# Performance work log

Hardware: AMD Instinct MI355X
Metric: run time of the kernel (lower is better)

Reference implementation:

```python
import jax, jax.numpy as jnp
import numpy as np

N, L, E_Q, E_TOTAL, H, FORECAST = 4, 2048, 512, 512, 8, 8
E_HEAD = E_TOTAL // H
DT = 1.0
NEG = -1e30


def setup_inputs() -> dict:
    rng = jax.random.key(0)
    ks = jax.random.split(rng, 8)
    inv = 1.0 / np.sqrt(E_Q)
    return {
        "query": jax.random.normal(ks[0], (N, L, E_Q), jnp.float32),
        "key": jax.random.normal(ks[1], (N, L, E_Q), jnp.float32),
        "value": jax.random.normal(ks[2], (N, L, E_Q), jnp.float32),
        "Wqkv": jax.random.normal(ks[3], (E_Q, 3 * E_TOTAL), jnp.float32) * inv,
        "bqkv": jnp.zeros((3 * E_TOTAL,), jnp.float32),
        "Wo": jax.random.normal(ks[4], (E_TOTAL, E_Q), jnp.float32) * (1.0 / np.sqrt(E_TOTAL)),
        "bo": jnp.zeros((E_Q,), jnp.float32),
        "Xi": jax.random.normal(ks[5], (H, E_HEAD, E_HEAD), jnp.float32) * 0.02,
    }


def reference(query, key, value, Wqkv, bqkv, Wo, bo, Xi):
    # NOTE: original forward projects `query` into q,k,v (key/value args unused).
    b, s, _ = query.shape
    qkv = query @ Wqkv + bqkv                      # [b, s, 3E]
    q, k, v = jnp.split(qkv, 3, axis=-1)
    split_heads = lambda t: t.reshape(b, s, H, E_HEAD).transpose(0, 2, 1, 3)  # [b,H,s,h]
    q, k, v = split_heads(q), split_heads(k), split_heads(v)
    # causal SDPA
    scale = 1.0 / np.sqrt(E_HEAD)
    scores = jnp.einsum('bhqd,bhkd->bhqk', q, k) * scale
    causal = jnp.tril(jnp.ones((s, s), bool))
    scores = jnp.where(causal, scores, NEG)
    probs = jax.nn.softmax(scores, axis=-1)
    attn = jnp.einsum('bhqk,bhkd->bhqd', probs, v)  # [b,H,s,h]
    # per-head SINDy linear dynamics, strict symmetry -> skew-symmetric A
    A = Xi - jnp.swapaxes(Xi, -1, -2)               # [H,h,h]

    def step(x, _):
        x2 = x + DT * jnp.einsum('bhsd,hde->bhse', x, A)
        return x2, x2

    _, ys = jax.lax.scan(step, attn, None, length=FORECAST)  # [n,b,H,s,h]
    roll = jnp.transpose(ys, (1, 0, 3, 2, 4)).reshape(b, FORECAST, s, E_TOTAL)
    return roll @ Wo + bo                            # [b, n, s, E_q]
```

## Files before the change

### kernel.cpp

```cpp
#include <hip/hip_runtime.h>
#include <math.h>


#define NEGV -1e30f

typedef __bf16 bf16_t;
typedef __bf16 bf16x4 __attribute__((ext_vector_type(4)));
typedef __bf16 bf16x8 __attribute__((ext_vector_type(8)));
typedef float f32x4 __attribute__((ext_vector_type(4)));

#define MFMA(a, b, c) __builtin_amdgcn_mfma_f32_16x16x32_bf16((a), (b), (c), 0, 0, 0)

#define QSCALE 0.18033688011112042f

__device__ __forceinline__ bf16x8* swz_ptr(bf16_t* base, int r, int cb) {
  return (bf16x8*)((char*)base + r * 128 + (cb ^ ((r & 7) << 4)));
}
__device__ __forceinline__ const bf16x8* swz_cptr(const bf16_t* base, int r, int cb) {
  return (const bf16x8*)((const char*)base + r * 128 + (cb ^ ((r & 7) << 4)));
}

__device__ __forceinline__ void gload16(const bf16_t* g, bf16_t* l) {
  __builtin_amdgcn_global_load_lds(
      (const __attribute__((address_space(1))) void*)g,
      (__attribute__((address_space(3))) void*)l, 16, 0, 0);
}


__global__ __launch_bounds__(256) void xconv(const float* __restrict__ X,
                                             bf16_t* __restrict__ Xb) {
  const int gid = blockIdx.x * 256 + threadIdx.x;
  const int s = gid >> 6, j = gid & 63;
  const float4* src = (const float4*)(X + (size_t)s * 512 + j * 8);
  const float4 f0 = src[0], f1 = src[1];
  bf16x8 v;
  v[0] = (bf16_t)f0.x; v[1] = (bf16_t)f0.y; v[2] = (bf16_t)f0.z; v[3] = (bf16_t)f0.w;
  v[4] = (bf16_t)f1.x; v[5] = (bf16_t)f1.y; v[6] = (bf16_t)f1.z; v[7] = (bf16_t)f1.w;
  *(bf16x8*)&Xb[(size_t)s * 512 + (j >> 3) * 64 + 8 * ((j & 7) ^ (s & 7))] = v;
}

__global__ __launch_bounds__(256) void wconv(const float* __restrict__ W,
                                             bf16_t* __restrict__ WT) {
  const int n0 = blockIdx.x * 64, k0 = blockIdx.y * 64;
  __shared__ float Wf[64][65];
  const int tid = threadIdx.x;
#pragma unroll
  for (int c = 0; c < 16; ++c) {
    const int idx = tid + c * 256;
    const int kk = idx >> 6, nn = idx & 63;
    Wf[kk][nn] = W[(size_t)(k0 + kk) * 1536 + n0 + nn];
  }
  __syncthreads();
  const int nr = tid >> 2;
  const int jb = (tid & 3) * 2;
#pragma unroll
  for (int t = 0; t < 2; ++t) {
    const int j = jb + t;
    bf16x8 v;
#pragma unroll
    for (int i = 0; i < 8; ++i) v[i] = (bf16_t)Wf[j * 8 + i][nr];
    *(bf16x8*)&WT[(size_t)(n0 + nr) * 512 + k0 + 8 * (j ^ (nr & 7))] = v;
  }
}

__global__ __launch_bounds__(256) void build_powers(const float* __restrict__ Xi,
                                                    float* __restrict__ pows) {
  const int h = blockIdx.x;
  __shared__ __align__(16) float P[64][68];
  __shared__ __align__(16) float cur[64][68];
  const int tid = threadIdx.x;
  const float* xi = Xi + (size_t)h * 4096;
  float* dst = pows + (size_t)h * 8 * 4096;
  for (int idx = tid; idx < 4096; idx += 256) {
    const int i = idx >> 6, j = idx & 63;
    const float p = (i == j ? 1.f : 0.f) + xi[i * 64 + j] - xi[j * 64 + i];
    P[i][j] = p;
    cur[i][j] = p;
    dst[idx] = p;
  }
  __syncthreads();
  const int i = tid >> 2;
  const int j0 = (tid & 3) * 16;
  for (int n = 1; n < 8; ++n) {
    float a[16];
#pragma unroll
    for (int jj = 0; jj < 16; ++jj) a[jj] = 0.f;
    for (int dd = 0; dd < 64; ++dd) {
      const float c = cur[i][dd];
#pragma unroll
      for (int jj = 0; jj < 16; ++jj) a[jj] += c * P[dd][j0 + jj];
    }
    __syncthreads();
#pragma unroll
    for (int jj = 0; jj < 16; ++jj) {
      cur[i][j0 + jj] = a[jj];
      dst[n * 4096 + i * 64 + j0 + jj] = a[jj];
    }
    __syncthreads();
  }
}

__global__ __launch_bounds__(256) void build_B(const float* __restrict__ pows,
                                               const float* __restrict__ Wo,
                                               bf16_t* __restrict__ BmatT) {
  const int et = blockIdx.x;
  const int n = blockIdx.y;
  const int h = blockIdx.z;
  __shared__ __align__(16) float P[64][68];
  __shared__ __align__(16) float We[64][128];
  const int tid = threadIdx.x;
  const float* src = pows + ((size_t)h * 8 + n) * 4096;
  for (int idx = tid; idx < 4096; idx += 256) P[idx >> 6][idx & 63] = src[idx];
  const int e0 = et * 128;
  for (int idx = tid; idx < 8192; idx += 256) {
    const int dd = idx >> 7, e = idx & 127;
    We[dd][e] = Wo[(size_t)(h * 64 + dd) * 512 + e0 + e];
  }
  __syncthreads();
  const int d = tid >> 2;
  const int eq = (tid & 3) * 32;
  float acc[32];
#pragma unroll
  for (int j = 0; j < 32; ++j) acc[j] = 0.f;
  for (int dd = 0; dd < 64; ++dd) {
    const float p = P[d][dd];
#pragma unroll
    for (int j = 0; j < 32; ++j) acc[j] += p * We[dd][eq + j];
  }
  bf16_t* dst = BmatT + (size_t)n * 512 * 512 + (size_t)(e0 + eq) * 512 + h * 64;
  const int dlo = d & 7, dhi = d >> 3;
#pragma unroll
  for (int j = 0; j < 32; ++j)
    dst[(size_t)j * 512 + 8 * (dhi ^ (j & 7)) + dlo] = (bf16_t)acc[j];
}

__global__ __launch_bounds__(256) void qkv_gemm(const bf16_t* __restrict__ Xb,
                                                const bf16_t* __restrict__ WT,
                                                const float* __restrict__ bias,
                                                bf16_t* __restrict__ qw,
                                                bf16_t* __restrict__ kw,
                                                bf16_t* __restrict__ vt) {
  __shared__ __align__(16) bf16_t As[128 * 64];
  __shared__ __align__(16) bf16_t Bs[128 * 64];
  const int tid = threadIdx.x;
  const int wave = tid >> 6, lane = tid & 63;
  const int g = lane >> 4, li = lane & 15;
  const int row0 = blockIdx.x * 128;
  const int col0 = blockIdx.y * 128;
  const int wm = (wave >> 1) * 64, wn = (wave & 1) * 64;
  f32x4 acc[4][4] = {};
  const bf16_t* asrc = Xb + (size_t)(row0 + wave * 32 + (lane >> 3)) * 512 + (lane & 7) * 8;
  const bf16_t* bsrc = WT + (size_t)(col0 + wave * 32 + (lane >> 3)) * 512 + (lane & 7) * 8;
  bf16_t* adst = &As[wave * 32 * 64];
  bf16_t* bdst = &Bs[wave * 32 * 64];
  for (int k0 = 0; k0 < 512; k0 += 64) {
#pragma unroll
    for (int c = 0; c < 4; ++c) {
      gload16(asrc + (size_t)c * 8 * 512 + k0, adst + c * 512);
      gload16(bsrc + (size_t)c * 8 * 512 + k0, bdst + c * 512);
    }
    __syncthreads();
#pragma unroll
    for (int ks = 0; ks < 2; ++ks) {
      bf16x8 af[4], bfr[4];
#pragma unroll
      for (int mr = 0; mr < 4; ++mr)
        af[mr] = *swz_cptr(As, wm + mr * 16 + li, ks * 64 + g * 16);
#pragma unroll
      for (int nr = 0; nr < 4; ++nr)
        bfr[nr] = *swz_cptr(Bs, wn + nr * 16 + li, ks * 64 + g * 16);
#pragma unroll
      for (int mr = 0; mr < 4; ++mr)
#pragma unroll
        for (int nr = 0; nr < 4; ++nr)
          acc[mr][nr] = MFMA(af[mr], bfr[nr], acc[mr][nr]);
    }
    __syncthreads();
  }
  const int cbase = col0 + wn;
  const int sel = cbase >> 9;
  const int hh = (cbase & 511) >> 6;
  const int bb = row0 >> 11;
  const size_t hb = (size_t)(bb * 8 + hh) * (2048 * 64);
  if (sel == 2) {
    bf16_t* vbase = vt + hb;
#pragma unroll
    for (int nr = 0; nr < 4; ++nr) {
      const int dcol = nr * 16 + li;
      const float bv = bias[cbase + dcol];
#pragma unroll
      for (int mr = 0; mr < 4; ++mr) {
        bf16x4 pk;
#pragma unroll
        for (int i = 0; i < 4; ++i) pk[i] = (bf16_t)(acc[mr][nr][i] + bv);
        const int s = (row0 + wm + mr * 16 + g * 4) & 2047;
        *(bf16x4*)&vbase[(size_t)dcol * 2048 + s] = pk;
      }
    }
  } else {
    bf16_t* dstp = (sel == 0 ? qw : kw) + hb;
    const float sc = (sel == 0) ? QSCALE : 1.0f;
#pragma unroll
    for (int nr = 0; nr < 4; ++nr) {
      const int dcol = nr * 16 + li;
      const float bv = bias[cbase + dcol];
#pragma unroll
      for (int mr = 0; mr < 4; ++mr) {
#pragma unroll
        for (int i = 0; i < 4; ++i) {
          const int r = row0 + wm + mr * 16 + g * 4 + i;
          const int s = r & 2047;
          dstp[(size_t)s * 64 + dcol] = (bf16_t)((acc[mr][nr][i] + bv) * sc);
        }
      }
    }
  }
}

__global__ __launch_bounds__(256) void fattn(const bf16_t* __restrict__ qw,
                                             const bf16_t* __restrict__ kw,
                                             const bf16_t* __restrict__ vt,
                                             bf16_t* __restrict__ attn,
                                             float* __restrict__ opart,
                                             float* __restrict__ ml) {
  __shared__ __align__(16) bf16_t Ks[2][64][64];
  __shared__ __align__(16) bf16_t Vs[2][64][64];
  __shared__ __align__(16) bf16_t Ps[4][16][64];
  const int tid = threadIdx.x;
  const int w = tid >> 6;
  const int lane = tid & 63;
  const int g = lane >> 4;
  const int li = lane & 15;
  const int x = blockIdx.x;
  int qt, ktb, kte, chunk;
  bool split;
  if (x < 16) {
    qt = 31 - x; ktb = 0; kte = 16; chunk = 0; split = true;
  } else if (x < 32) {
    qt = 47 - x; ktb = 16; kte = qt + 1; chunk = 1; split = true;
  } else {
    qt = 47 - x; ktb = 0; kte = qt + 1; chunk = 0; split = false;
  }
  const int h = blockIdx.y;
  const int b = blockIdx.z;
  const size_t base = ((size_t)(b * 8 + h)) * (2048 * 64);
  const int q0 = qt * 64;
  const int qrow = q0 + w * 16 + li;
  const bf16x8 aq0 = *(const bf16x8*)(qw + base + (size_t)qrow * 64 + g * 8);
  const bf16x8 aq1 = *(const bf16x8*)(qw + base + (size_t)qrow * 64 + 32 + g * 8);
  const bf16_t* kbase = kw + base;
  const bf16_t* vbase = vt + base;
  const int r_st = tid >> 2;
  const int qu = tid & 3;
  {
    const bf16_t* kp = kbase + (size_t)(ktb * 64 + r_st) * 64 + qu * 16;
    const bf16_t* vp = vbase + (size_t)r_st * 2048 + ktb * 64 + qu * 16;
    *swz_ptr(&Ks[0][0][0], r_st, qu * 32) = *(const bf16x8*)kp;
    *swz_ptr(&Ks[0][0][0], r_st, qu * 32 + 16) = *(const bf16x8*)(kp + 8);
    *swz_ptr(&Vs[0][0][0], r_st, qu * 32) = *(const bf16x8*)vp;
    *swz_ptr(&Vs[0][0][0], r_st, qu * 32 + 16) = *(const bf16x8*)(vp + 8);
  }
  f32x4 accO[4] = {};
  float m_run = -__builtin_inff();
  float l_run = 0.f;
  char* const psrow = (char*)&Ps[w][li][0];
  const int pswz = (li & 7) << 4;
  for (int kt = ktb; kt < kte; ++kt) {
    __syncthreads();
    const int cur = (kt - ktb) & 1;
    const bool pf = (kt + 1) < kte;
    bf16x8 nk0, nk1, nv0, nv1;
    if (pf) {
      const int kb2 = (kt + 1) * 64;
      const bf16_t* kp = kbase + (size_t)(kb2 + r_st) * 64 + qu * 16;
      const bf16_t* vp = vbase + (size_t)r_st * 2048 + kb2 + qu * 16;
      nk0 = *(const bf16x8*)kp;
      nk1 = *(const bf16x8*)(kp + 8);
      nv0 = *(const bf16x8*)vp;
      nv1 = *(const bf16x8*)(vp + 8);
    }
    f32x4 sv[4];
    __builtin_amdgcn_s_setprio(1);
#pragma unroll
    for (int nt = 0; nt < 4; ++nt) {
      const bf16x8 bk0 = *swz_cptr(&Ks[cur][0][0], nt * 16 + li, g * 16);
      const bf16x8 bk1 = *swz_cptr(&Ks[cur][0][0], nt * 16 + li, 64 + g * 16);
      f32x4 z = {0.f, 0.f, 0.f, 0.f};
      z = MFMA(bk0, aq0, z);
      sv[nt] = MFMA(bk1, aq1, z);
    }
    __builtin_amdgcn_s_setprio(0);
    if (kt == qt) {
#pragma unroll
      for (int nt = 0; nt < 4; ++nt)
#pragma unroll
        for (int i = 0; i < 4; ++i)
          if (nt * 16 + g * 4 + i > w * 16 + li) sv[nt][i] = NEGV;
    }
    float pmax = sv[0][0];
#pragma unroll
    for (int nt = 0; nt < 4; ++nt)
#pragma unroll
      for (int i = 0; i < 4; ++i) pmax = fmaxf(pmax, sv[nt][i]);
    pmax = fmaxf(pmax, __shfl_xor(pmax, 16, 64));
    pmax = fmaxf(pmax, __shfl_xor(pmax, 32, 64));
    if (!__all(pmax - m_run <= 8.f)) {
      const float newm = fmaxf(m_run, pmax);
      const float sc = exp2f(m_run - newm);
      l_run *= sc;
      m_run = newm;
#pragma unroll
      for (int nt = 0; nt < 4; ++nt)
#pragma unroll
        for (int i = 0; i < 4; ++i) accO[nt][i] *= sc;
    }
    float rsum = 0.f;
#pragma unroll
    for (int nt = 0; nt < 4; ++nt) {
#pragma unroll
      for (int i = 0; i < 4; ++i) {
        const float p = exp2f(sv[nt][i] - m_run);
        sv[nt][i] = p;
        rsum += p;
      }
    }
    rsum += __shfl_xor(rsum, 16, 64);
    rsum += __shfl_xor(rsum, 32, 64);
    l_run += rsum;
#pragma unroll
    for (int nt = 0; nt < 4; ++nt) {
      bf16x4 pk;
#pragma unroll
      for (int i = 0; i < 4; ++i) pk[i] = (bf16_t)sv[nt][i];
      *(bf16x4*)(psrow + ((nt * 32 + g * 8) ^ pswz)) = pk;
    }
    const bf16x8 ap0 = *(const bf16x8*)(psrow + ((g * 16) ^ pswz));
    const bf16x8 ap1 = *(const bf16x8*)(psrow + ((64 + g * 16) ^ pswz));
    __builtin_amdgcn_s_setprio(1);
#pragma unroll
    for (int nt = 0; nt < 4; ++nt) {
      const bf16x8 bv0 = *swz_cptr(&Vs[cur][0][0], nt * 16 + li, g * 16);
      const bf16x8 bv1 = *swz_cptr(&Vs[cur][0][0], nt * 16 + li, 64 + g * 16);
      accO[nt] = MFMA(bv0, ap0, accO[nt]);
      accO[nt] = MFMA(bv1, ap1, accO[nt]);
    }
    __builtin_amdgcn_s_setprio(0);
    if (pf) {
      *swz_ptr(&Ks[cur ^ 1][0][0], r_st, qu * 32) = nk0;
      *swz_ptr(&Ks[cur ^ 1][0][0], r_st, qu * 32 + 16) = nk1;
      *swz_ptr(&Vs[cur ^ 1][0][0], r_st, qu * 32) = nv0;
      *swz_ptr(&Vs[cur ^ 1][0][0], r_st, qu * 32 + 16) = nv1;
    }
  }
  if (!split) {
    const float inv = 1.0f / l_run;
    bf16_t* arow = attn + (size_t)(b * 2048 + qrow) * 512 + h * 64;
#pragma unroll
    for (int nt = 0; nt < 4; ++nt) {
      bf16x4 pk;
#pragma unroll
      for (int i = 0; i < 4; ++i) pk[i] = (bf16_t)(accO[nt][i] * inv);
      *(bf16x4*)&arow[8 * ((nt * 2 + (g >> 1)) ^ (li & 7)) + (g & 1) * 4] = pk;
    }
  } else {
    const int row = w * 16 + li;
    const size_t pbase = (((size_t)(b * 8 + h) * 16 + (qt - 16)) * 2 + chunk) * 64 + row;
    float* op = opart + pbase * 64;
#pragma unroll
    for (int nt = 0; nt < 4; ++nt) *(f32x4*)&op[nt * 16 + g * 4] = accO[nt];
    if (g == 0) {
      ml[pbase * 2] = m_run;
      ml[pbase * 2 + 1] = l_run;
    }
  }
}

__global__ __launch_bounds__(256) void fcombine(const float* __restrict__ opart,
                                                const float* __restrict__ ml,
                                                bf16_t* __restrict__ attn) {
  const int qi = blockIdx.x;
  const int h = blockIdx.y;
  const int b = blockIdx.z;
  const int tid = threadIdx.x;
  const int row = tid >> 2;
  const int dq = (tid & 3) * 16;
  const size_t base2 = ((size_t)(b * 8 + h) * 16 + qi) * 2;
  const size_t p0 = (base2 * 64 + row);
  const size_t p1 = ((base2 + 1) * 64 + row);
  const float m1 = ml[p0 * 2], l1 = ml[p0 * 2 + 1];
  const float m2 = ml[p1 * 2], l2 = ml[p1 * 2 + 1];
  const float m = fmaxf(m1, m2);
  const float w1 = exp2f(m1 - m), w2 = exp2f(m2 - m);
  const float inv = 1.0f / (l1 * w1 + l2 * w2);
  const float* o1 = opart + p0 * 64;
  const float* o2 = opart + p1 * 64;
  const int qrow = (16 + qi) * 64 + row;
  bf16_t* arow = attn + (size_t)(b * 2048 + qrow) * 512 + h * 64;
#pragma unroll
  for (int t = 0; t < 2; ++t) {
    const int c0 = dq + t * 8;
    const f32x4 a1 = *(const f32x4*)&o1[c0];
    const f32x4 b1 = *(const f32x4*)&o1[c0 + 4];
    const f32x4 a2 = *(const f32x4*)&o2[c0];
    const f32x4 b2 = *(const f32x4*)&o2[c0 + 4];
    bf16x8 v;
#pragma unroll
    for (int i = 0; i < 4; ++i) {
      v[i] = (bf16_t)((a1[i] * w1 + a2[i] * w2) * inv);
      v[4 + i] = (bf16_t)((b1[i] * w1 + b2[i] * w2) * inv);
    }
    *(bf16x8*)&arow[8 * ((c0 >> 3) ^ (row & 7))] = v;
  }
}

__global__ __launch_bounds__(256, 2) void out_gemm(const bf16_t* __restrict__ A,
                                                   const bf16_t* __restrict__ BmatT,
                                                   const float* __restrict__ bo,
                                                   float* __restrict__ out) {
  __shared__ __align__(16) bf16_t As[128 * 64];
  __shared__ __align__(16) bf16_t Bs[2][128 * 64];
  const int tid = threadIdx.x;
  const int wave = tid >> 6, lane = tid & 63;
  const int g = lane >> 4, li = lane & 15;
  const int row0 = blockIdx.x * 128;
  const int col0 = blockIdx.y * 128;
  const int nf0 = blockIdx.z * 2;
  const int wm = (wave >> 1) * 64, wn = (wave & 1) * 64;
  f32x4 acc[2][4][4] = {};
  const bf16_t* asrc = A + (size_t)(row0 + wave * 32 + (lane >> 3)) * 512 + (lane & 7) * 8;
  const bf16_t* bsrc = BmatT + (size_t)nf0 * 512 * 512 +
                       (size_t)(col0 + wave * 32 + (lane >> 3)) * 512 + (lane & 7) * 8;
  bf16_t* adst = &As[wave * 32 * 64];
  bf16_t* bdst0 = &Bs[0][wave * 32 * 64];
  bf16_t* bdst1 = &Bs[1][wave * 32 * 64];
  for (int k0 = 0; k0 < 512; k0 += 64) {
#pragma unroll
    for (int c = 0; c < 4; ++c) {
      gload16(asrc + (size_t)c * 8 * 512 + k0, adst + c * 512);
      gload16(bsrc + (size_t)c * 8 * 512 + k0, bdst0 + c * 512);
      gload16(bsrc + 262144 + (size_t)c * 8 * 512 + k0, bdst1 + c * 512);
    }
    __syncthreads();
#pragma unroll
    for (int ks = 0; ks < 2; ++ks) {
      bf16x8 af[4];
#pragma unroll
      for (int mr = 0; mr < 4; ++mr)
        af[mr] = *swz_cptr(As, wm + mr * 16 + li, ks * 64 + g * 16);
#pragma unroll
      for (int f = 0; f < 2; ++f) {
        bf16x8 bfr[4];
#pragma unroll
        for (int nr = 0; nr < 4; ++nr)
          bfr[nr] = *swz_cptr(Bs[f], wn + nr * 16 + li, ks * 64 + g * 16);
#pragma unroll
        for (int mr = 0; mr < 4; ++mr)
#pragma unroll
          for (int nr = 0; nr < 4; ++nr)
            acc[f][mr][nr] = MFMA(af[mr], bfr[nr], acc[f][mr][nr]);
      }
    }
    __syncthreads();
  }
  const int bb = row0 >> 11;
#pragma unroll
  for (int f = 0; f < 2; ++f) {
    float* obase = out + ((size_t)(bb * 8 + nf0 + f)) * (2048 * 512);
#pragma unroll
    for (int nr = 0; nr < 4; ++nr) {
      const int c = col0 + wn + nr * 16 + li;
      const float bv = bo[c];
#pragma unroll
      for (int mr = 0; mr < 4; ++mr) {
#pragma unroll
        for (int i = 0; i < 4; ++i) {
          const int r = row0 + wm + mr * 16 + g * 4 + i;
          const int s = r & 2047;
          obase[(size_t)s * 512 + c] = acc[f][mr][nr][i] + bv;
        }
      }
    }
  }
}

extern "C" void kernel_launch(void* const* d_in, const int* in_sizes, int n_in,
                              void* d_out, int out_size, void* d_ws, size_t ws_size,
                              hipStream_t stream) {
  const float* query = (const float*)d_in[0];
  const float* Wqkv = (const float*)d_in[3];
  const float* bqkv = (const float*)d_in[4];
  const float* Wo = (const float*)d_in[5];
  const float* bo = (const float*)d_in[6];
  const float* Xi = (const float*)d_in[7];
  float* out = (float*)d_out;

  char* ws = (char*)d_ws;
  bf16_t* qw = (bf16_t*)(ws + 0);
  bf16_t* kw = (bf16_t*)(ws + 8388608);
  bf16_t* vt = (bf16_t*)(ws + 16777216);
  bf16_t* Xb = (bf16_t*)(ws + 25165824);
  bf16_t* attn = (bf16_t*)(ws + 25165824);
  bf16_t* BmatT = (bf16_t*)(ws + 33554432);
  float* pows = (float*)(ws + 37748736);
  bf16_t* WT = (bf16_t*)(ws + 38797312);
  float* opart = (float*)(ws + 40370176);
  float* mlbuf = (float*)(ws + 57147392);

  xconv<<<dim3(2048), dim3(256), 0, stream>>>(query, Xb);
  wconv<<<dim3(24, 8), dim3(256), 0, stream>>>(Wqkv, WT);
  build_powers<<<dim3(8), dim3(256), 0, stream>>>(Xi, pows);
  build_B<<<dim3(4, 8, 8), dim3(256), 0, stream>>>(pows, Wo, BmatT);
  qkv_gemm<<<dim3(64, 12), dim3(256), 0, stream>>>(Xb, WT, bqkv, qw, kw, vt);
  fattn<<<dim3(48, 8, 4), dim3(256), 0, stream>>>(qw, kw, vt, attn, opart, mlbuf);
  fcombine<<<dim3(16, 8, 4), dim3(256), 0, stream>>>(opart, mlbuf, attn);
  out_gemm<<<dim3(64, 4, 4), dim3(256), 0, stream>>>(attn, BmatT, bo, out);
}
```

Before: 185.5 us.

## Double-buffer LDS tiles in qkv and output GEMMs, one forecast step per block

Both GEMMs now use two LDS buffers and prefetch the next K tile with async global-to-LDS loads while the current tile feeds the MFMAs. Explicit vmcnt waits and raw barriers replace __syncthreads. The output GEMM no longer computes two forecast steps per block: each block handles one, so the grid doubles along z and the A tile is loaded twice as often. The aim is to hide global load latency and cut per-thread accumulator pressure, at the cost of more LDS per block and extra A traffic.

```diff
diff --git a/kernel.cpp b/kernel.cpp
--- a/kernel.cpp
+++ b/kernel.cpp
@@ -140,8 +140,8 @@
                                                 bf16_t* __restrict__ qw,
                                                 bf16_t* __restrict__ kw,
                                                 bf16_t* __restrict__ vt) {
-  __shared__ __align__(16) bf16_t As[128 * 64];
-  __shared__ __align__(16) bf16_t Bs[128 * 64];
+  __shared__ __align__(16) bf16_t As[2][128 * 64];
+  __shared__ __align__(16) bf16_t Bs[2][128 * 64];
   const int tid = threadIdx.x;
   const int wave = tid >> 6, lane = tid & 63;
   const int g = lane >> 4, li = lane & 15;
@@ -151,31 +151,49 @@
   f32x4 acc[4][4] = {};
   const bf16_t* asrc = Xb + (size_t)(row0 + wave * 32 + (lane >> 3)) * 512 + (lane & 7) * 8;
   const bf16_t* bsrc = WT + (size_t)(col0 + wave * 32 + (lane >> 3)) * 512 + (lane & 7) * 8;
-  bf16_t* adst = &As[wave * 32 * 64];
-  bf16_t* bdst = &Bs[wave * 32 * 64];
-  for (int k0 = 0; k0 < 512; k0 += 64) {
+  bf16_t* adst0 = &As[0][wave * 32 * 64];
+  bf16_t* adst1 = &As[1][wave * 32 * 64];
+  bf16_t* bdst0 = &Bs[0][wave * 32 * 64];
+  bf16_t* bdst1 = &Bs[1][wave * 32 * 64];
+  auto stage = [&](int bi, int kt) {
+    const int k0 = kt * 64;
+    bf16_t* ad = bi ? adst1 : adst0;
+    bf16_t* bd = bi ? bdst1 : bdst0;
 #pragma unroll
     for (int c = 0; c < 4; ++c) {
-      gload16(asrc + (size_t)c * 8 * 512 + k0, adst + c * 512);
-      gload16(bsrc + (size_t)c * 8 * 512 + k0, bdst + c * 512);
-    }
-    __syncthreads();
+      gload16(asrc + (size_t)c * 8 * 512 + k0, ad + c * 512);
+      gload16(bsrc + (size_t)c * 8 * 512 + k0, bd + c * 512);
+    }
+  };
+  stage(0, 0);
+#pragma unroll
+  for (int t = 0; t < 8; ++t) {
+    const int cur = t & 1;
+    if (t < 7) {
+      stage(cur ^ 1, t + 1);
+      asm volatile("s_waitcnt vmcnt(8)" ::: "memory");
+    } else {
+      asm volatile("s_waitcnt vmcnt(0)" ::: "memory");
+    }
+    __builtin_amdgcn_s_barrier();
+    __builtin_amdgcn_sched_barrier(0);
 #pragma unroll
     for (int ks = 0; ks < 2; ++ks) {
       bf16x8 af[4], bfr[4];
 #pragma unroll
       for (int mr = 0; mr < 4; ++mr)
-        af[mr] = *swz_cptr(As, wm + mr * 16 + li, ks * 64 + g * 16);
+        af[mr] = *swz_cptr(As[cur], wm + mr * 16 + li, ks * 64 + g * 16);
 #pragma unroll
       for (int nr = 0; nr < 4; ++nr)
-        bfr[nr] = *swz_cptr(Bs, wn + nr * 16 + li, ks * 64 + g * 16);
+        bfr[nr] = *swz_cptr(Bs[cur], wn + nr * 16 + li, ks * 64 + g * 16);
 #pragma unroll
       for (int mr = 0; mr < 4; ++mr)
 #pragma unroll
         for (int nr = 0; nr < 4; ++nr)
           acc[mr][nr] = MFMA(af[mr], bfr[nr], acc[mr][nr]);
     }
-    __syncthreads();
+    __builtin_amdgcn_s_barrier();
+    __builtin_amdgcn_sched_barrier(0);
   }
   const int cbase = col0 + wn;
   const int sel = cbase >> 9;
@@ -413,71 +431,80 @@
   }
 }
 
-__global__ __launch_bounds__(256, 2) void out_gemm(const bf16_t* __restrict__ A,
-                                                   const bf16_t* __restrict__ BmatT,
-                                                   const float* __restrict__ bo,
-                                                   float* __restrict__ out) {
-  __shared__ __align__(16) bf16_t As[128 * 64];
+__global__ __launch_bounds__(256) void out_gemm(const bf16_t* __restrict__ A,
+                                                const bf16_t* __restrict__ BmatT,
+                                                const float* __restrict__ bo,
+                                                float* __restrict__ out) {
+  __shared__ __align__(16) bf16_t As[2][128 * 64];
   __shared__ __align__(16) bf16_t Bs[2][128 * 64];
   const int tid = threadIdx.x;
   const int wave = tid >> 6, lane = tid & 63;
   const int g = lane >> 4, li = lane & 15;
   const int row0 = blockIdx.x * 128;
   const int col0 = blockIdx.y * 128;
-  const int nf0 = blockIdx.z * 2;
+  const int nf = blockIdx.z;
   const int wm = (wave >> 1) * 64, wn = (wave & 1) * 64;
-  f32x4 acc[2][4][4] = {};
+  f32x4 acc[4][4] = {};
   const bf16_t* asrc = A + (size_t)(row0 + wave * 32 + (lane >> 3)) * 512 + (lane & 7) * 8;
-  const bf16_t* bsrc = BmatT + (size_t)nf0 * 512 * 512 +
+  const bf16_t* bsrc = BmatT + (size_t)nf * 512 * 512 +
                        (size_t)(col0 + wave * 32 + (lane >> 3)) * 512 + (lane & 7) * 8;
-  bf16_t* adst = &As[wave * 32 * 64];
+  bf16_t* adst0 = &As[0][wave * 32 * 64];
+  bf16_t* adst1 = &As[1][wave * 32 * 64];
   bf16_t* bdst0 = &Bs[0][wave * 32 * 64];
   bf16_t* bdst1 = &Bs[1][wave * 32 * 64];
-  for (int k0 = 0; k0 < 512; k0 += 64) {
+  auto stage = [&](int bi, int kt) {
+    const int k0 = kt * 64;
+    bf16_t* ad = bi ? adst1 : adst0;
+    bf16_t* bd = bi ? bdst1 : bdst0;
 #pragma unroll
     for (int c = 0; c < 4; ++c) {
-      gload16(asrc + (size_t)c * 8 * 512 + k0, adst + c * 512);
-      gload16(bsrc + (size_t)c * 8 * 512 + k0, bdst0 + c * 512);
-      gload16(bsrc + 262144 + (size_t)c * 8 * 512 + k0, bdst1 + c * 512);
-    }
-    __syncthreads();
+      gload16(asrc + (size_t)c * 8 * 512 + k0, ad + c * 512);
+      gload16(bsrc + (size_t)c * 8 * 512 + k0, bd + c * 512);
+    }
+  };
+  stage(0, 0);
+#pragma unroll
+  for (int t = 0; t < 8; ++t) {
+    const int cur = t & 1;
+    if (t < 7) {
+      stage(cur ^ 1, t + 1);
+      asm volatile("s_waitcnt vmcnt(8)" ::: "memory");
+    } else {
+      asm volatile("s_waitcnt vmcnt(0)" ::: "memory");
+    }
+    __builtin_amdgcn_s_barrier();
+    __builtin_amdgcn_sched_barrier(0);
 #pragma unroll
     for (int ks = 0; ks < 2; ++ks) {
-      bf16x8 af[4];
+      bf16x8 af[4], bfr[4];
 #pragma unroll
       for (int mr = 0; mr < 4; ++mr)
-        af[mr] = *swz_cptr(As, wm + mr * 16 + li, ks * 64 + g * 16);
-#pragma unroll
-      for (int f = 0; f < 2; ++f) {
-        bf16x8 bfr[4];
+        af[mr] = *swz_cptr(As[cur], wm + mr * 16 + li, ks * 64 + g * 16);
+#pragma unroll
+      for (int nr = 0; nr < 4; ++nr)
+        bfr[nr] = *swz_cptr(Bs[cur], wn + nr * 16 + li, ks * 64 + g * 16);
+#pragma unroll
+      for (int mr = 0; mr < 4; ++mr)
 #pragma unroll
         for (int nr = 0; nr < 4; ++nr)
-          bfr[nr] = *swz_cptr(Bs[f], wn + nr * 16 + li, ks * 64 + g * 16);
-#pragma unroll
-        for (int mr = 0; mr < 4; ++mr)
-#pragma unroll
-          for (int nr = 0; nr < 4; ++nr)
-            acc[f][mr][nr] = MFMA(af[mr], bfr[nr], acc[f][mr][nr]);
-      }
-    }
-    __syncthreads();
+          acc[mr][nr] = MFMA(af[mr], bfr[nr], acc[mr][nr]);
+    }
+    __builtin_amdgcn_s_barrier();
+    __builtin_amdgcn_sched_barrier(0);
   }
   const int bb = row0 >> 11;
-#pragma unroll
-  for (int f = 0; f < 2; ++f) {
-    float* obase = out + ((size_t)(bb * 8 + nf0 + f)) * (2048 * 512);
-#pragma unroll
-    for (int nr = 0; nr < 4; ++nr) {
-      const int c = col0 + wn + nr * 16 + li;
-      const float bv = bo[c];
-#pragma unroll
-      for (int mr = 0; mr < 4; ++mr) {
-#pragma unroll
-        for (int i = 0; i < 4; ++i) {
-          const int r = row0 + wm + mr * 16 + g * 4 + i;
-          const int s = r & 2047;
-          obase[(size_t)s * 512 + c] = acc[f][mr][nr][i] + bv;
-        }
+  float* obase = out + ((size_t)(bb * 8 + nf)) * (2048 * 512);
+#pragma unroll
+  for (int nr = 0; nr < 4; ++nr) {
+    const int c = col0 + wn + nr * 16 + li;
+    const float bv = bo[c];
+#pragma unroll
+    for (int mr = 0; mr < 4; ++mr) {
+#pragma unroll
+      for (int i = 0; i < 4; ++i) {
+        const int r = row0 + wm + mr * 16 + g * 4 + i;
+        const int s = r & 2047;
+        obase[(size_t)s * 512 + c] = acc[mr][nr][i] + bv;
       }
     }
   }
@@ -513,5 +540,5 @@
   qkv_gemm<<<dim3(64, 12), dim3(256), 0, stream>>>(Xb, WT, bqkv, qw, kw, vt);
   fattn<<<dim3(48, 8, 4), dim3(256), 0, stream>>>(qw, kw, vt, attn, opart, mlbuf);
   fcombine<<<dim3(16, 8, 4), dim3(256), 0, stream>>>(opart, mlbuf, attn);
-  out_gemm<<<dim3(64, 4, 4), dim3(256), 0, stream>>>(attn, BmatT, bo, out);
-}
+  out_gemm<<<dim3(64, 4, 8), dim3(256), 0, stream>>>(attn, BmatT, bo, out);
+}
```

Measured after the change: 183.7 us. No clear change (-0.9%).
